# Kernel tuning notes

Hardware: AMD Instinct MI355X
Metric: run time of the kernel (lower is better)

Reference implementation:

```python
import jax, jax.numpy as jnp
import numpy as np

LSTM = 400      # lstm_size
K_ATT = 10      # attention_mixture_components
M_OUT = 20      # output_mixture_components
ALPHA = 60      # alphabet_size
B, T, TC = 64, 600, 50


def setup_inputs() -> dict:
    key = jax.random.key(0)
    ks = jax.random.split(key, 16)
    s = 0.05  # weight init scale to keep activations sane
    rn = lambda k, shape: (jax.random.normal(k, shape, jnp.float32) * s)
    d1 = 3 + ALPHA                # lstm1 input: [window, x]
    d2 = 3 + LSTM + ALPHA         # lstm2 input: [x, h1, window]
    d3 = 3 + 2 * LSTM + ALPHA     # lstm3 input: [x, h1, h2, window]
    H4 = 4 * LSTM
    return {
        "inputs": jax.random.normal(ks[0], (B, T, 3), jnp.float32),
        "char_seq": jax.random.randint(ks[1], (B, TC), 0, ALPHA),
        "char_seq_lengths": jax.random.randint(ks[2], (B,), 1, TC + 1),
        "W_ih1": rn(ks[3], (H4, d1)), "b_ih1": jnp.zeros((H4,), jnp.float32),
        "W_hh1": rn(ks[4], (H4, LSTM)), "b_hh1": jnp.zeros((H4,), jnp.float32),
        "W_ih2": rn(ks[5], (H4, d2)), "b_ih2": jnp.zeros((H4,), jnp.float32),
        "W_hh2": rn(ks[6], (H4, LSTM)), "b_hh2": jnp.zeros((H4,), jnp.float32),
        "W_ih3": rn(ks[7], (H4, d3)), "b_ih3": jnp.zeros((H4,), jnp.float32),
        "W_hh3": rn(ks[8], (H4, LSTM)), "b_hh3": jnp.zeros((H4,), jnp.float32),
        "W_att": rn(ks[9], (3 * K_ATT, LSTM)), "b_att": jnp.zeros((3 * K_ATT,), jnp.float32),
        "W_gmm": rn(ks[10], (6 * M_OUT + 1, 3 * LSTM)), "b_gmm": jnp.zeros((6 * M_OUT + 1,), jnp.float32),
    }


def _lstm_cell(x, h, c, Wih, bih, Whh, bhh):
    # torch.nn.LSTMCell gate order: i, f, g, o
    g = x @ Wih.T + bih + h @ Whh.T + bhh
    i, f, gg, o = jnp.split(g, 4, axis=-1)
    c_new = jax.nn.sigmoid(f) * c + jax.nn.sigmoid(i) * jnp.tanh(gg)
    h_new = jax.nn.sigmoid(o) * jnp.tanh(c_new)
    return h_new, c_new


def reference(inputs, char_seq, char_seq_lengths,
              W_ih1, b_ih1, W_hh1, b_hh1,
              W_ih2, b_ih2, W_hh2, b_hh2,
              W_ih3, b_ih3, W_hh3, b_hh3,
              W_att, b_att, W_gmm, b_gmm):
    M = M_OUT
    char_oh = jax.nn.one_hot(char_seq, ALPHA, dtype=inputs.dtype)       # [B,TC,A]
    u = jnp.arange(TC, dtype=inputs.dtype)                              # [TC]
    len_mask = (u[None, :] < char_seq_lengths[:, None].astype(inputs.dtype)).astype(inputs.dtype)  # [B,TC]

    def step(carry, x_t):
        h1, c1, h2, c2, h3, c3, window, kappa = carry
        # lstm1([window, x])
        h1, c1 = _lstm_cell(jnp.concatenate([window, x_t], -1), h1, c1, W_ih1, b_ih1, W_hh1, b_hh1)
        # Graves Gaussian-mixture attention window (no softmax)
        p = jnp.exp(h1 @ W_att.T + b_att)                               # [B,3K]
        alpha, beta, dkappa = jnp.split(p, 3, axis=-1)
        kappa = kappa + dkappa                                          # [B,K]
        diff = kappa[:, :, None] - u[None, None, :]                     # [B,K,TC]
        phi = jnp.sum(alpha[:, :, None] * jnp.exp(-beta[:, :, None] * diff * diff), axis=1)  # [B,TC]
        phi = phi * len_mask
        window = jnp.einsum('bt,bta->ba', phi, char_oh)                 # [B,A]
        # lstm2([x, h1, window]) / lstm3([x, h1, h2, window])
        h2, c2 = _lstm_cell(jnp.concatenate([x_t, h1, window], -1), h2, c2, W_ih2, b_ih2, W_hh2, b_hh2)
        h3, c3 = _lstm_cell(jnp.concatenate([x_t, h1, h2, window], -1), h3, c3, W_ih3, b_ih3, W_hh3, b_hh3)
        # GMM output layer (bias=None -> 0)
        z = jnp.concatenate([h1, h2, h3], -1) @ W_gmm.T + b_gmm          # [B,6M+1]
        e_hat = z[:, :1]
        pi_hat = z[:, 1:1 + M]
        mus = z[:, 1 + M:1 + 3 * M]
        sig_hat = z[:, 1 + 3 * M:1 + 5 * M]
        rho_hat = z[:, 1 + 5 * M:1 + 6 * M]
        out = jnp.concatenate([
            jax.nn.softmax(pi_hat, axis=-1),   # pis   [B,M]
            mus,                               # mus   [B,2M]
            jnp.exp(sig_hat),                  # sigmas[B,2M]
            jnp.tanh(rho_hat),                 # rhos  [B,M]
            jax.nn.sigmoid(e_hat),             # es    [B,1]
        ], axis=-1)
        return (h1, c1, h2, c2, h3, c3, window, kappa), out

    z0 = jnp.zeros((B, LSTM), inputs.dtype)
    carry0 = (z0, z0, z0, z0, z0, z0,
              jnp.zeros((B, ALPHA), inputs.dtype),
              jnp.zeros((B, K_ATT), inputs.dtype))
    _, outs = jax.lax.scan(step, carry0, jnp.swapaxes(inputs, 0, 1))    # [T,B,6M+1]
    return jnp.transpose(outs, (1, 0, 2))                               # [B,T,6M+1]
```

## Files before the change

### kernel.cpp

```cpp
#include <hip/hip_runtime.h>
#include <hip/hip_bf16.h>

#define NB 64
#define NT 600
#define NTC 50
#define NH 400
#define NKATT 10
#define NALPHA 60
#define NOUT 121

typedef unsigned short u16;
typedef _Float16 f16x2 __attribute__((ext_vector_type(2)));
typedef _Float16 f16x4 __attribute__((ext_vector_type(4)));
typedef _Float16 f16x8 __attribute__((ext_vector_type(8)));

#if defined(__has_builtin)
#if __has_builtin(__builtin_amdgcn_fdot2)
#define FDOT2(a,b,c) __builtin_amdgcn_fdot2((a),(b),(c),false)
#endif
#endif
#ifndef FDOT2
#define FDOT2(a,b,c) ((c) + (float)(a)[0]*(float)(b)[0] + (float)(a)[1]*(float)(b)[1])
#endif

#define ROWSP 1664

#define T1N 13
#define CGRP 15

#define H1R 0
#define H2R 102400
#define H3R 204800
#define WINR 256000
#define ST_FLOATS 271360
#define SLOT_H 25600
#define SLOT_W 3840

#define OF_WATT 0
#define OF_INB1 25600
#define OF_INB2 33792
#define OF_ACCS 48128
#define OF_AB   52736
#define OF_PHI  53696
#define OF_KAP  55296
#define OF_CHS  55616
#define OF_LEN  57216
#define OF_C1   57248
#define OF_C2   58272
#define SMEM_TOTAL 59296

__device__ __align__(16) f16x2 g_WT1[256 * ROWSP];
__device__ __align__(16) f16x2 g_WT2[448 * ROWSP];
__device__ __align__(16) f16x2 g_WT3[640 * ROWSP];
__device__ __align__(16) f16x2 g_WG8[150 * 128 * 4];
__device__ __align__(16) f16x2 g_WattP[200 * 32];
__device__ __align__(16) float g_fb1[ROWSP], g_fb2[ROWSP], g_fb3[ROWSP];
__device__ float g_batt[30], g_bgmm[121];
__device__ __align__(16) float g_inp[115200];
__device__ __align__(16) float g_state[ST_FLOATS];
__device__ unsigned int g_cnt[8 * 4 * 32];
__device__ int g_isf32;

#define CNT_A 0
#define CNT_B 1
#define CNT_C 2

__device__ __forceinline__ float bf2f(u16 v) {
    union { unsigned int u; float f; } t; t.u = ((unsigned int)v) << 16; return t.f;
}
__device__ __forceinline__ u16 f2bf(float f) {
    union { float ff; unsigned int u; } t; t.ff = f;
    unsigned int lsb = (t.u >> 16) & 1u;
    t.u += 0x7fffu + lsb;
    return (u16)(t.u >> 16);
}
__device__ __forceinline__ float sigm(float x) { return 1.f / (1.f + expf(-x)); }
__device__ __forceinline__ f16x2 packpair(float a, float b) {
    f16x2 r; r[0] = (_Float16)a; r[1] = (_Float16)b; return r;
}

__device__ __forceinline__ void st_agent(float* p, float v) {
    __hip_atomic_store(p, v, __ATOMIC_RELAXED, __HIP_MEMORY_SCOPE_AGENT);
}
__device__ __forceinline__ float2 ld2_agent(const float* p) {
    unsigned long long u = __hip_atomic_load((const unsigned long long*)p,
                                             __ATOMIC_RELAXED, __HIP_MEMORY_SCOPE_AGENT);
    union { unsigned long long u; float2 f; } t; t.u = u; return t.f;
}
__device__ __forceinline__ unsigned ld_cnt(int bg, int cid) {
    return __hip_atomic_load(&g_cnt[(bg * 4 + cid) * 32], __ATOMIC_RELAXED, __HIP_MEMORY_SCOPE_AGENT);
}
__device__ __forceinline__ void cnt_bump(int bg, int cid) {
    if (threadIdx.x == 0)
        __hip_atomic_fetch_add(&g_cnt[(bg * 4 + cid) * 32], 1u, __ATOMIC_RELAXED, __HIP_MEMORY_SCOPE_AGENT);
}
__device__ __forceinline__ void cnt_wait(int bg, int cid, unsigned tgt) {
    if (threadIdx.x == 0 && tgt > 0) {
        while (ld_cnt(bg, cid) < tgt) __builtin_amdgcn_s_sleep(1);
    }
    __syncthreads();
}

__global__ void k_detect(const void* whh1) {
    if (threadIdx.x == 0 && blockIdx.x == 0) {
        const u16* p = (const u16*)whh1;
        int f32 = 0;
        for (int k = 0; k < 256; ++k) {
            float v = bf2f(p[2 * k]);
            if (!(fabsf(v) < 1e3f)) f32 = 1;
        }
        g_isf32 = f32;
    }
}

__global__ void k_convert(const void* inp,
                          const void* wih1, const void* bih1, const void* whh1, const void* bhh1,
                          const void* wih2, const void* bih2, const void* whh2, const void* bhh2,
                          const void* wih3, const void* bih3, const void* whh3, const void* bhh3,
                          const void* watt, const void* batt, const void* wgmm, const void* bgmm)
{
    const int gt = blockIdx.x * blockDim.x + threadIdx.x;
    const int gs = gridDim.x * blockDim.x;
    const int f32 = g_isf32;
    auto ld = [f32](const void* p, int i) -> float {
        return f32 ? ((const float*)p)[i] : bf2f(((const u16*)p)[i]);
    };
    auto w1col = [&](int kf, int row) -> float {
        if (kf < 400) return ld(whh1, row * 400 + kf);
        if (kf < 460) return ld(wih1, row * 63 + (kf - 400));
        if (kf < 463) return ld(wih1, row * 63 + 60 + (kf - 460));
        return 0.f;
    };
    auto w2col = [&](int kf, int row) -> float {
        if (kf < 400) return ld(wih2, row * 463 + 3 + kf);
        if (kf < 800) return ld(whh2, row * 400 + (kf - 400));
        if (kf < 860) return ld(wih2, row * 463 + 403 + (kf - 800));
        if (kf < 863) return ld(wih2, row * 463 + (kf - 860));
        return 0.f;
    };
    auto w3col = [&](int kf, int row) -> float {
        if (kf < 400)  return ld(wih3, row * 863 + 3 + kf);
        if (kf < 800)  return ld(wih3, row * 863 + 403 + (kf - 400));
        if (kf < 1200) return ld(whh3, row * 400 + (kf - 800));
        if (kf < 1260) return ld(wih3, row * 863 + 803 + (kf - 1200));
        if (kf < 1263) return ld(wih3, row * 863 + (kf - 1260));
        return 0.f;
    };
    for (int i = gt; i < 256 * ROWSP; i += gs) {
        int k2 = i / ROWSP, rp = i % ROWSP;
        int j = rp >> 2, g = rp & 3;
        float a = 0.f, b = 0.f;
        if (j < 400) { int row = g * 400 + j; a = w1col(2 * k2, row); b = w1col(2 * k2 + 1, row); }
        g_WT1[i] = packpair(a, b);
    }
    for (int i = gt; i < 448 * ROWSP; i += gs) {
        int k2 = i / ROWSP, rp = i % ROWSP;
        int j = rp >> 2, g = rp & 3;
        float a = 0.f, b = 0.f;
        if (j < 400) { int row = g * 400 + j; a = w2col(2 * k2, row); b = w2col(2 * k2 + 1, row); }
        g_WT2[i] = packpair(a, b);
    }
    for (int i = gt; i < 640 * ROWSP; i += gs) {
        int k2 = i / ROWSP, rp = i % ROWSP;
        int j = rp >> 2, g = rp & 3;
        float a = 0.f, b = 0.f;
        if (j < 400) { int row = g * 400 + j; a = w3col(2 * k2, row); b = w3col(2 * k2 + 1, row); }
        g_WT3[i] = packpair(a, b);
    }
    for (int i = gt; i < ROWSP; i += gs) {
        int j = i >> 2, g = i & 3;
        float b1 = 0.f, b2 = 0.f, b3 = 0.f;
        if (j < 400) {
            int row = g * 400 + j;
            b1 = ld(bih1, row) + ld(bhh1, row);
            b2 = ld(bih2, row) + ld(bhh2, row);
            b3 = ld(bih3, row) + ld(bhh3, row);
        }
        g_fb1[i] = b1; g_fb2[i] = b2; g_fb3[i] = b3;
    }
    for (int i = gt; i < 200 * 32; i += gs) {
        int k2 = i / 32, r = i % 32;
        float a = 0.f, b = 0.f;
        if (r < 30) { a = ld(watt, r * 400 + 2 * k2); b = ld(watt, r * 400 + 2 * k2 + 1); }
        g_WattP[i] = packpair(a, b);
    }
    for (int i = gt; i < 150 * 128 * 4; i += gs) {
        int k8 = i >> 9, rem = i & 511, r = rem >> 2, j = rem & 3;
        int kp = k8 * 4 + j;
        float a = 0.f, b = 0.f;
        if (r < 121) { a = ld(wgmm, r * 1200 + 2 * kp); b = ld(wgmm, r * 1200 + 2 * kp + 1); }
        g_WG8[i] = packpair(a, b);
    }
    for (int i = gt; i < 30; i += gs)  g_batt[i] = ld(batt, i);
    for (int i = gt; i < 121; i += gs) g_bgmm[i] = ld(bgmm, i);
    for (int i = gt; i < 115200; i += gs) g_inp[i] = ld(inp, i);
    for (int i = gt; i < ST_FLOATS; i += gs) g_state[i] = 0.f;
    for (int i = gt; i < 8 * 4 * 32; i += gs) g_cnt[i] = 0u;
}

template<int KP2>
__device__ __forceinline__ void lstm_core(const f16x2* __restrict__ WT, const float* __restrict__ fb,
                                          float* __restrict__ cL, float* __restrict__ hdst,
                                          const f16x2* inb, float* accS, int rg, int bg, int tid)
{
    const int wv = tid >> 6, lane = tid & 63;
    const int ck4 = KP2 >> 5;
    const int k40 = wv * ck4;
    const int rbase = rg * 128 + lane * 2;
    float acc[2][8];
    #pragma unroll
    for (int r = 0; r < 2; ++r)
        #pragma unroll
        for (int b = 0; b < 8; ++b) acc[r][b] = 0.f;
    const f16x2* wp = WT + (size_t)(k40 * 4) * ROWSP + rbase;
    #pragma unroll 2
    for (int k4 = 0; k4 < ck4; ++k4) {
        f16x2 wa[4], wb[4];
        #pragma unroll
        for (int j = 0; j < 4; ++j) {
            union { f16x4 v; f16x2 p[2]; } u;
            u.v = *(const f16x4*)(wp + (size_t)j * ROWSP);
            wa[j] = u.p[0]; wb[j] = u.p[1];
        }
        #pragma unroll
        for (int b = 0; b < 8; ++b) {
            union { f16x8 v; f16x2 p[4]; } h;
            h.v = *(const f16x8*)(inb + b * KP2 + (k40 + k4) * 4);
            #pragma unroll
            for (int j = 0; j < 4; ++j) {
                acc[0][b] = FDOT2(wa[j], h.p[j], acc[0][b]);
                acc[1][b] = FDOT2(wb[j], h.p[j], acc[1][b]);
            }
        }
        wp += 4 * ROWSP;
    }
    #pragma unroll
    for (int r = 0; r < 2; ++r)
        #pragma unroll
        for (int b = 0; b < 8; ++b)
            atomicAdd(&accS[(lane * 2 + r) * 9 + b], acc[r][b]);
    __syncthreads();
    if (tid < 256) {
        int bl = tid >> 5, jj = tid & 31;
        int j = rg * 32 + jj;
        if (j < 400) {
            int rl = jj * 4;
            float gi = accS[(rl + 0) * 9 + bl] + fb[rg * 128 + rl + 0];
            float gf = accS[(rl + 1) * 9 + bl] + fb[rg * 128 + rl + 1];
            float gg = accS[(rl + 2) * 9 + bl] + fb[rg * 128 + rl + 2];
            float go = accS[(rl + 3) * 9 + bl] + fb[rg * 128 + rl + 3];
            float c = cL[bl * 32 + jj];
            float cn = sigm(gf) * c + sigm(gi) * tanhf(gg);
            cL[bl * 32 + jj] = cn;
            st_agent(&hdst[(bg * 8 + bl) * 400 + j], sigm(go) * tanhf(cn));
        }
    }
}

__device__ void out_head(void* out, int t, int obid, int tid, char* smem)
{
    f16x2* zb = (f16x2*)smem;
    float* zv = (float*)(smem + 9600);
    const float* h1 = g_state + H1R + (t & 3) * SLOT_H;
    const float* h2 = g_state + H2R + (t & 3) * SLOT_H;
    const float* h3 = g_state + H3R + (t & 1) * SLOT_H;
    for (int i = tid; i < 4 * 600; i += 512) {
        int bq = i / 600, p = i % 600; int b = obid * 4 + bq;
        int kf = 2 * p;
        const float* src = (kf < 400) ? (h1 + b * 400 + kf)
                         : (kf < 800) ? (h2 + b * 400 + (kf - 400))
                                      : (h3 + b * 400 + (kf - 800));
        float2 hv = ld2_agent(src);
        zb[bq * 600 + p] = packpair(hv.x, hv.y);
    }
    __syncthreads();
    {
        int bq = tid >> 7, r = tid & 127;
        float ac0 = (r < 121) ? g_bgmm[r] : 0.f, ac1 = 0.f, ac2 = 0.f, ac3 = 0.f;
        const f16x8* zp = (const f16x8*)(zb + bq * 600);
        #pragma unroll 4
        for (int k8 = 0; k8 < 150; ++k8) {
            union { f16x8 v; f16x2 p[4]; } w, z;
            w.v = *(const f16x8*)&g_WG8[(k8 * 128 + r) * 4];
            z.v = zp[k8];
            ac0 = FDOT2(w.p[0], z.p[0], ac0);
            ac1 = FDOT2(w.p[1], z.p[1], ac1);
            ac2 = FDOT2(w.p[2], z.p[2], ac2);
            ac3 = FDOT2(w.p[3], z.p[3], ac3);
        }
        if (r < 121) zv[bq * 121 + r] = (ac0 + ac1) + (ac2 + ac3);
    }
    __syncthreads();
    if (tid < 484) {
        int bl = tid / 121, jo = tid - bl * 121;
        const float* z = zv + bl * 121;
        float val;
        if (jo < 20) {
            float m = -1e30f;
            for (int i = 0; i < 20; ++i) m = fmaxf(m, z[1 + i]);
            float s = 0.f;
            for (int i = 0; i < 20; ++i) s += expf(z[1 + i] - m);
            val = expf(z[1 + jo] - m) / s;
        } else if (jo < 60)  val = z[jo + 1];
        else if (jo < 100)   val = expf(z[jo + 1]);
        else if (jo < 120)   val = tanhf(z[jo + 1]);
        else                 val = 1.f / (1.f + expf(-z[0]));
        int idx = ((obid * 4 + bl) * NT + t) * NOUT + jo;
        if (g_isf32) ((float*)out)[idx] = val;
        else         ((u16*)out)[idx]  = f2bf(val);
    }
    __syncthreads();
}

__global__ __launch_bounds__(512) void k_persist(void* out,
                                                 const int* __restrict__ cseq,
                                                 const int* __restrict__ clen)
{
    __shared__ __align__(16) char smem[SMEM_TOTAL];
    const int tid = threadIdx.x;
    const int bid = blockIdx.x;
    const int x = bid & 7, s = bid >> 3;
    int role, rg = 0, bg = 0, obid = 0;
    if (s < 8)       { role = 0; rg = x; bg = s; }
    else if (s < 13) { role = 0; int q = 5 * x + (s - 8);  rg = 8 + (q >> 3); bg = q & 7; }
    else if (s < 21) { role = 1; rg = x; bg = s - 13; }
    else if (s < 26) { role = 1; int q = 5 * x + (s - 21); rg = 8 + (q >> 3); bg = q & 7; }
    else             { role = 2; obid = 2 * x + (s - 26); bg = x; }

    if (role == 0) {
        f16x2* wattL = (f16x2*)(smem + OF_WATT);
        f16x2* inb1 = (f16x2*)(smem + OF_INB1);
        f16x2* inb2 = (f16x2*)(smem + OF_INB2);
        float* accS = (float*)(smem + OF_ACCS);
        float* ab  = (float*)(smem + OF_AB);
        float* phi = (float*)(smem + OF_PHI);
        float* kap = (float*)(smem + OF_KAP);
        int* chs = (int*)(smem + OF_CHS);
        int* len = (int*)(smem + OF_LEN);
        float* c1 = (float*)(smem + OF_C1);
        float* c2 = (float*)(smem + OF_C2);

        for (int i = tid; i < 200 * 32; i += 512) wattL[i] = g_WattP[i];
        for (int i = tid; i < 8 * 256; i += 512) inb1[i] = packpair(0.f, 0.f);
        for (int i = tid; i < 8 * 448; i += 512) inb2[i] = packpair(0.f, 0.f);
        for (int i = tid; i < 1152; i += 512) accS[i] = 0.f;
        if (tid < 80) kap[tid] = 0.f;
        if (tid >= 128 && tid < 384) { c1[tid - 128] = 0.f; c2[tid - 128] = 0.f; }
        for (int i = tid; i < 400; i += 512) chs[i] = cseq[(bg * 8 + i / 50) * NTC + i % 50];
        if (tid >= 384 && tid < 392) len[tid - 384] = clen[bg * 8 + (tid - 384)];
        if (tid < 16) {
            int bl = tid >> 1, hh = tid & 1, b = bg * 8 + bl;
            if (hh == 0) inb1[bl * 256 + 230] = packpair(g_inp[(b * NT) * 3 + 0], g_inp[(b * NT) * 3 + 1]);
            else         inb1[bl * 256 + 231] = packpair(g_inp[(b * NT) * 3 + 2], 0.f);
        }
        __syncthreads();
        lstm_core<256>(g_WT1, g_fb1, c1, g_state + H1R + 0 * SLOT_H, inb1, accS, rg, bg, tid);
        __syncthreads();
        cnt_bump(bg, CNT_A);

        for (int t = 0; t <= NT; ++t) {
            if (t >= 1) {
                for (int i = tid; i < 8 * 230; i += 512) {
                    int bl = i / 230, p = i - bl * 230;
                    inb2[bl * 448 + (p < 200 ? p : p + 200)] = inb1[bl * 256 + p];
                }
                if (tid < 16) {
                    int bl = tid >> 1, hh = tid & 1, b = bg * 8 + bl;
                    if (hh == 0) inb2[bl * 448 + 430] = packpair(g_inp[(b * NT + t - 1) * 3 + 0], g_inp[(b * NT + t - 1) * 3 + 1]);
                    else         inb2[bl * 448 + 431] = packpair(g_inp[(b * NT + t - 1) * 3 + 2], 0.f);
                }
                for (int i = tid; i < 1152; i += 512) accS[i] = 0.f;
                cnt_wait(bg, CNT_B, 13u * (unsigned)(t - 1));
                const float* h2s = g_state + H2R + ((t - 2) & 3) * SLOT_H;
                for (int i = tid; i < 8 * 200; i += 512) {
                    int bl = i / 200, p = i - bl * 200, b = bg * 8 + bl;
                    float2 hv = ld2_agent(h2s + b * 400 + 2 * p);
                    inb2[bl * 448 + 200 + p] = packpair(hv.x, hv.y);
                }
                __syncthreads();
                lstm_core<448>(g_WT2, g_fb2, c2, g_state + H2R + ((t - 1) & 3) * SLOT_H, inb2, accS, rg, bg, tid);
                __syncthreads();
                cnt_bump(bg, CNT_B);
                if (t == NT) break;
            }
            if (tid == 0) {
                unsigned tgtA = 13u * (unsigned)(t + 1);
                while (ld_cnt(bg, CNT_A) < tgtA) __builtin_amdgcn_s_sleep(1);
                if (t >= 2) {
                    unsigned tgtC = 15u * (unsigned)(t - 1);
                    while (ld_cnt(bg, CNT_C) < tgtC) __builtin_amdgcn_s_sleep(1);
                }
            }
            __syncthreads();
            const float* h1s = g_state + H1R + (t & 3) * SLOT_H;
            for (int i = tid; i < 8 * 200; i += 512) {
                int bl = i / 200, p = i - bl * 200, b = bg * 8 + bl;
                float2 hv = ld2_agent(h1s + b * 400 + 2 * p);
                inb1[bl * 256 + p] = packpair(hv.x, hv.y);
            }
            __syncthreads();
            if (tid < 240) {
                int bl = tid / 30, rr = tid - bl * 30;
                float a0 = g_batt[rr], a1 = 0.f;
                const f16x2* hp = inb1 + bl * 256;
                #pragma unroll 4
                for (int k2 = 0; k2 < 200; k2 += 2) {
                    a0 = FDOT2(wattL[(k2 + 0) * 32 + rr], hp[k2 + 0], a0);
                    a1 = FDOT2(wattL[(k2 + 1) * 32 + rr], hp[k2 + 1], a1);
                }
                ab[bl * 30 + rr] = expf(a0 + a1);
            }
            __syncthreads();
            if (tid < 400) {
                int bl = tid / 50, u = tid - bl * 50;
                float ph = 0.f;
                if (u < len[bl]) {
                    float uf = (float)u;
                    for (int k = 0; k < 10; ++k) {
                        float kn = kap[bl * 10 + k] + ab[bl * 30 + 20 + k];
                        float d = kn - uf;
                        ph += ab[bl * 30 + k] * expf(-ab[bl * 30 + 10 + k] * d * d);
                    }
                }
                phi[bl * 50 + u] = ph;
            }
            __syncthreads();
            if (tid < 240) {
                int bl = tid / 30, q = tid - bl * 30;
                int a0i = 2 * q, a1i = 2 * q + 1;
                float w0 = 0.f, w1 = 0.f;
                for (int u = 0; u < NTC; ++u) {
                    float pv = phi[bl * 50 + u]; int cc = chs[bl * 50 + u];
                    if (cc == a0i) w0 += pv;
                    if (cc == a1i) w1 += pv;
                }
                inb1[bl * 256 + 200 + q] = packpair(w0, w1);
                if (rg == 0) {
                    float* wr = g_state + WINR + (t & 3) * SLOT_W + (bg * 8 + bl) * 60;
                    st_agent(wr + a0i, w0); st_agent(wr + a1i, w1);
                }
            } else if (tid >= 256 && tid < 336) {
                int i = tid - 256; int bl = i / 10, k = i - bl * 10;
                kap[bl * 10 + k] += ab[bl * 30 + 20 + k];
            }
            if (t + 1 < NT && tid < 16) {
                int bl = tid >> 1, hh = tid & 1, b = bg * 8 + bl;
                if (hh == 0) inb1[bl * 256 + 230] = packpair(g_inp[(b * NT + t + 1) * 3 + 0], g_inp[(b * NT + t + 1) * 3 + 1]);
                else         inb1[bl * 256 + 231] = packpair(g_inp[(b * NT + t + 1) * 3 + 2], 0.f);
            }
            __syncthreads();
            if (t + 1 < NT) {
                for (int i = tid; i < 1152; i += 512) accS[i] = 0.f;
                __syncthreads();
                lstm_core<256>(g_WT1, g_fb1, c1, g_state + H1R + ((t + 1) & 3) * SLOT_H, inb1, accS, rg, bg, tid);
                __syncthreads();
                cnt_bump(bg, CNT_A);
            }
        }
    } else if (role == 1) {
        f16x2* inb3 = (f16x2*)smem;
        float* accS = (float*)(smem + 20480);
        float* c3 = (float*)(smem + 25088);
        for (int i = tid; i < 8 * 640; i += 512) inb3[i] = packpair(0.f, 0.f);
        if (tid < 256) c3[tid] = 0.f;
        __syncthreads();
        for (int t = 0; t < NT; ++t) {
            if (tid < 16) {
                int bl = tid >> 1, hh = tid & 1, b = bg * 8 + bl;
                if (hh == 0) inb3[bl * 640 + 630] = packpair(g_inp[(b * NT + t) * 3 + 0], g_inp[(b * NT + t) * 3 + 1]);
                else         inb3[bl * 640 + 631] = packpair(g_inp[(b * NT + t) * 3 + 2], 0.f);
            }
            for (int i = tid; i < 1152; i += 512) accS[i] = 0.f;
            cnt_wait(bg, CNT_B, 13u * (unsigned)(t + 1));
            const float* h1s = g_state + H1R + (t & 3) * SLOT_H;
            const float* h2s = g_state + H2R + (t & 3) * SLOT_H;
            const float* h3s = g_state + H3R + ((t - 1) & 1) * SLOT_H;
            const float* ws  = g_state + WINR + (t & 3) * SLOT_W;
            for (int i = tid; i < 8 * 630; i += 512) {
                int bl = i / 630, p = i - bl * 630, b = bg * 8 + bl;
                const float* src = (p < 200) ? h1s + b * 400 + 2 * p
                                 : (p < 400) ? h2s + b * 400 + 2 * (p - 200)
                                 : (p < 600) ? h3s + b * 400 + 2 * (p - 400)
                                             : ws  + b * 60  + 2 * (p - 600);
                float2 hv = ld2_agent(src);
                inb3[bl * 640 + p] = packpair(hv.x, hv.y);
            }
            __syncthreads();
            lstm_core<640>(g_WT3, g_fb3, c3, g_state + H3R + (t & 1) * SLOT_H, inb3, accS, rg, bg, tid);
            __syncthreads();
            cnt_bump(bg, CNT_C);
            cnt_wait(bg, CNT_C, 15u * (unsigned)(t + 1));
        }
    } else {
        for (int t = 0; t < NT; ++t) {
            cnt_bump(bg, CNT_C);
            cnt_wait(bg, CNT_C, 15u * (unsigned)(t + 1));
            out_head(out, t, obid, tid, smem);
        }
    }
}

extern "C" void kernel_launch(void* const* d_in, const int* in_sizes, int n_in,
                              void* d_out, int out_size, void* d_ws, size_t ws_size,
                              hipStream_t stream)
{
    hipLaunchKernelGGL(k_detect, dim3(1), dim3(64), 0, stream, d_in[5]);
    hipLaunchKernelGGL(k_convert, dim3(2048), dim3(256), 0, stream,
                       d_in[0],
                       d_in[3], d_in[4], d_in[5], d_in[6],
                       d_in[7], d_in[8], d_in[9], d_in[10],
                       d_in[11], d_in[12], d_in[13], d_in[14],
                       d_in[15], d_in[16], d_in[17], d_in[18]);
    void* outp = d_out;
    const int* cseq = (const int*)d_in[1];
    const int* clen = (const int*)d_in[2];
    void* args[] = { (void*)&outp, (void*)&cseq, (void*)&clen };
    hipLaunchCooperativeKernel((void*)k_persist, dim3(224), dim3(512), args, 0, stream);
}
```

Baseline: 25.31 ms.

## Move LSTM2 to role-1 blocks and recompute attention window redundantly

Role-0 blocks now run only LSTM1 plus attention. Role-1 blocks run LSTM2 and LSTM3 in sequence, recomputing the attention window locally instead of reading it from global memory. The h3 buffer widens to four slots, and role 1 drops its wait on the output head, so stages are more decoupled and LSTM1 can run further ahead. The cost is duplicated attention work in every role-1 block (which reads W_att from global rather than shared memory), and each role-1 block now does two LSTM layers serially per step.

Result: slower. 32.16 ms (+27.1%).

```diff
diff --git a/kernel.cpp b/kernel.cpp
--- a/kernel.cpp
+++ b/kernel.cpp
@@ -25,29 +25,32 @@
 
 #define ROWSP 1664
 
-#define T1N 13
-#define CGRP 15
-
 #define H1R 0
 #define H2R 102400
 #define H3R 204800
-#define WINR 256000
-#define ST_FLOATS 271360
+#define ST_FLOATS 307200
 #define SLOT_H 25600
-#define SLOT_W 3840
-
-#define OF_WATT 0
-#define OF_INB1 25600
-#define OF_INB2 33792
-#define OF_ACCS 48128
-#define OF_AB   52736
-#define OF_PHI  53696
-#define OF_KAP  55296
-#define OF_CHS  55616
-#define OF_LEN  57216
-#define OF_C1   57248
-#define OF_C2   58272
-#define SMEM_TOTAL 59296
+
+#define OF1_WATT 0
+#define OF1_INB1 25600
+#define OF1_ACCS 33792
+#define OF1_AB   38400
+#define OF1_PHI  39360
+#define OF1_KAP  40960
+#define OF1_CHS  41280
+#define OF1_LEN  42880
+#define OF1_C1   42912
+#define OF2_INB2 0
+#define OF2_INB3 14336
+#define OF2_ACCS 34816
+#define OF2_AB   39424
+#define OF2_PHI  40384
+#define OF2_KAP  41984
+#define OF2_CHS  42304
+#define OF2_LEN  43904
+#define OF2_C2   43936
+#define OF2_C3   44960
+#define SMEM_TOTAL 46080
 
 __device__ __align__(16) f16x2 g_WT1[256 * ROWSP];
 __device__ __align__(16) f16x2 g_WT2[448 * ROWSP];
@@ -257,13 +260,61 @@
     }
 }
 
+template<int STR, int WOFF>
+__device__ __forceinline__ void att_window(const f16x2* __restrict__ watt,
+                                           f16x2* inb, float* ab, float* phi, float* kap,
+                                           const int* chs, const int* len, int tid)
+{
+    if (tid < 240) {
+        int bl = tid / 30, rr = tid - bl * 30;
+        float a0 = g_batt[rr], a1 = 0.f;
+        const f16x2* hp = inb + bl * STR;
+        #pragma unroll 4
+        for (int k2 = 0; k2 < 200; k2 += 2) {
+            a0 = FDOT2(watt[(k2 + 0) * 32 + rr], hp[k2 + 0], a0);
+            a1 = FDOT2(watt[(k2 + 1) * 32 + rr], hp[k2 + 1], a1);
+        }
+        ab[bl * 30 + rr] = expf(a0 + a1);
+    }
+    __syncthreads();
+    if (tid < 400) {
+        int bl = tid / 50, u = tid - bl * 50;
+        float ph = 0.f;
+        if (u < len[bl]) {
+            float uf = (float)u;
+            for (int k = 0; k < 10; ++k) {
+                float kn = kap[bl * 10 + k] + ab[bl * 30 + 20 + k];
+                float d = kn - uf;
+                ph += ab[bl * 30 + k] * expf(-ab[bl * 30 + 10 + k] * d * d);
+            }
+        }
+        phi[bl * 50 + u] = ph;
+    }
+    __syncthreads();
+    if (tid < 240) {
+        int bl = tid / 30, q = tid - bl * 30;
+        int a0i = 2 * q, a1i = 2 * q + 1;
+        float w0 = 0.f, w1 = 0.f;
+        for (int u = 0; u < NTC; ++u) {
+            float pv = phi[bl * 50 + u]; int cc = chs[bl * 50 + u];
+            if (cc == a0i) w0 += pv;
+            if (cc == a1i) w1 += pv;
+        }
+        inb[bl * STR + WOFF + q] = packpair(w0, w1);
+    } else if (tid >= 256 && tid < 336) {
+        int i = tid - 256; int bl = i / 10, k = i - bl * 10;
+        kap[bl * 10 + k] += ab[bl * 30 + 20 + k];
+    }
+    __syncthreads();
+}
+
 __device__ void out_head(void* out, int t, int obid, int tid, char* smem)
 {
     f16x2* zb = (f16x2*)smem;
     float* zv = (float*)(smem + 9600);
     const float* h1 = g_state + H1R + (t & 3) * SLOT_H;
     const float* h2 = g_state + H2R + (t & 3) * SLOT_H;
-    const float* h3 = g_state + H3R + (t & 1) * SLOT_H;
+    const float* h3 = g_state + H3R + (t & 3) * SLOT_H;
     for (int i = tid; i < 4 * 600; i += 512) {
         int bq = i / 600, p = i % 600; int b = obid * 4 + bq;
         int kf = 2 * p;
@@ -328,24 +379,21 @@
     else             { role = 2; obid = 2 * x + (s - 26); bg = x; }
 
     if (role == 0) {
-        f16x2* wattL = (f16x2*)(smem + OF_WATT);
-        f16x2* inb1 = (f16x2*)(smem + OF_INB1);
-        f16x2* inb2 = (f16x2*)(smem + OF_INB2);
-        float* accS = (float*)(smem + OF_ACCS);
-        float* ab  = (float*)(smem + OF_AB);
-        float* phi = (float*)(smem + OF_PHI);
-        float* kap = (float*)(smem + OF_KAP);
-        int* chs = (int*)(smem + OF_CHS);
-        int* len = (int*)(smem + OF_LEN);
-        float* c1 = (float*)(smem + OF_C1);
-        float* c2 = (float*)(smem + OF_C2);
+        f16x2* wattL = (f16x2*)(smem + OF1_WATT);
+        f16x2* inb1 = (f16x2*)(smem + OF1_INB1);
+        float* accS = (float*)(smem + OF1_ACCS);
+        float* ab  = (float*)(smem + OF1_AB);
+        float* phi = (float*)(smem + OF1_PHI);
+        float* kap = (float*)(smem + OF1_KAP);
+        int* chs = (int*)(smem + OF1_CHS);
+        int* len = (int*)(smem + OF1_LEN);
+        float* c1 = (float*)(smem + OF1_C1);
 
         for (int i = tid; i < 200 * 32; i += 512) wattL[i] = g_WattP[i];
         for (int i = tid; i < 8 * 256; i += 512) inb1[i] = packpair(0.f, 0.f);
-        for (int i = tid; i < 8 * 448; i += 512) inb2[i] = packpair(0.f, 0.f);
         for (int i = tid; i < 1152; i += 512) accS[i] = 0.f;
         if (tid < 80) kap[tid] = 0.f;
-        if (tid >= 128 && tid < 384) { c1[tid - 128] = 0.f; c2[tid - 128] = 0.f; }
+        if (tid >= 128 && tid < 384) c1[tid - 128] = 0.f;
         for (int i = tid; i < 400; i += 512) chs[i] = cseq[(bg * 8 + i / 50) * NTC + i % 50];
         if (tid >= 384 && tid < 392) len[tid - 384] = clen[bg * 8 + (tid - 384)];
         if (tid < 16) {
@@ -358,36 +406,18 @@
         __syncthreads();
         cnt_bump(bg, CNT_A);
 
-        for (int t = 0; t <= NT; ++t) {
-            if (t >= 1) {
-                for (int i = tid; i < 8 * 230; i += 512) {
-                    int bl = i / 230, p = i - bl * 230;
-                    inb2[bl * 448 + (p < 200 ? p : p + 200)] = inb1[bl * 256 + p];
-                }
-                if (tid < 16) {
-                    int bl = tid >> 1, hh = tid & 1, b = bg * 8 + bl;
-                    if (hh == 0) inb2[bl * 448 + 430] = packpair(g_inp[(b * NT + t - 1) * 3 + 0], g_inp[(b * NT + t - 1) * 3 + 1]);
-                    else         inb2[bl * 448 + 431] = packpair(g_inp[(b * NT + t - 1) * 3 + 2], 0.f);
-                }
-                for (int i = tid; i < 1152; i += 512) accS[i] = 0.f;
-                cnt_wait(bg, CNT_B, 13u * (unsigned)(t - 1));
-                const float* h2s = g_state + H2R + ((t - 2) & 3) * SLOT_H;
-                for (int i = tid; i < 8 * 200; i += 512) {
-                    int bl = i / 200, p = i - bl * 200, b = bg * 8 + bl;
-                    float2 hv = ld2_agent(h2s + b * 400 + 2 * p);
-                    inb2[bl * 448 + 200 + p] = packpair(hv.x, hv.y);
-                }
-                __syncthreads();
-                lstm_core<448>(g_WT2, g_fb2, c2, g_state + H2R + ((t - 1) & 3) * SLOT_H, inb2, accS, rg, bg, tid);
-                __syncthreads();
-                cnt_bump(bg, CNT_B);
-                if (t == NT) break;
-            }
+        for (int t = 0; t < NT; ++t) {
+            if (t + 1 < NT && tid < 16) {
+                int bl = tid >> 1, hh = tid & 1, b = bg * 8 + bl;
+                if (hh == 0) inb1[bl * 256 + 230] = packpair(g_inp[(b * NT + t + 1) * 3 + 0], g_inp[(b * NT + t + 1) * 3 + 1]);
+                else         inb1[bl * 256 + 231] = packpair(g_inp[(b * NT + t + 1) * 3 + 2], 0.f);
+            }
+            for (int i = tid; i < 1152; i += 512) accS[i] = 0.f;
             if (tid == 0) {
                 unsigned tgtA = 13u * (unsigned)(t + 1);
                 while (ld_cnt(bg, CNT_A) < tgtA) __builtin_amdgcn_s_sleep(1);
-                if (t >= 2) {
-                    unsigned tgtC = 15u * (unsigned)(t - 1);
+                if (t >= 3) {
+                    unsigned tgtC = 15u * (unsigned)(t - 2);
                     while (ld_cnt(bg, CNT_C) < tgtC) __builtin_amdgcn_s_sleep(1);
                 }
             }
@@ -399,97 +429,79 @@
                 inb1[bl * 256 + p] = packpair(hv.x, hv.y);
             }
             __syncthreads();
-            if (tid < 240) {
-                int bl = tid / 30, rr = tid - bl * 30;
-                float a0 = g_batt[rr], a1 = 0.f;
-                const f16x2* hp = inb1 + bl * 256;
-                #pragma unroll 4
-                for (int k2 = 0; k2 < 200; k2 += 2) {
-                    a0 = FDOT2(wattL[(k2 + 0) * 32 + rr], hp[k2 + 0], a0);
-                    a1 = FDOT2(wattL[(k2 + 1) * 32 + rr], hp[k2 + 1], a1);
-                }
-                ab[bl * 30 + rr] = expf(a0 + a1);
-            }
-            __syncthreads();
-            if (tid < 400) {
-                int bl = tid / 50, u = tid - bl * 50;
-                float ph = 0.f;
-                if (u < len[bl]) {
-                    float uf = (float)u;
-                    for (int k = 0; k < 10; ++k) {
-                        float kn = kap[bl * 10 + k] + ab[bl * 30 + 20 + k];
-                        float d = kn - uf;
-                        ph += ab[bl * 30 + k] * expf(-ab[bl * 30 + 10 + k] * d * d);
-                    }
-                }
-                phi[bl * 50 + u] = ph;
-            }
-            __syncthreads();
-            if (tid < 240) {
-                int bl = tid / 30, q = tid - bl * 30;
-                int a0i = 2 * q, a1i = 2 * q + 1;
-                float w0 = 0.f, w1 = 0.f;
-                for (int u = 0; u < NTC; ++u) {
-                    float pv = phi[bl * 50 + u]; int cc = chs[bl * 50 + u];
-                    if (cc == a0i) w0 += pv;
-                    if (cc == a1i) w1 += pv;
-                }
-                inb1[bl * 256 + 200 + q] = packpair(w0, w1);
-                if (rg == 0) {
-                    float* wr = g_state + WINR + (t & 3) * SLOT_W + (bg * 8 + bl) * 60;
-                    st_agent(wr + a0i, w0); st_agent(wr + a1i, w1);
-                }
-            } else if (tid >= 256 && tid < 336) {
-                int i = tid - 256; int bl = i / 10, k = i - bl * 10;
-                kap[bl * 10 + k] += ab[bl * 30 + 20 + k];
-            }
-            if (t + 1 < NT && tid < 16) {
-                int bl = tid >> 1, hh = tid & 1, b = bg * 8 + bl;
-                if (hh == 0) inb1[bl * 256 + 230] = packpair(g_inp[(b * NT + t + 1) * 3 + 0], g_inp[(b * NT + t + 1) * 3 + 1]);
-                else         inb1[bl * 256 + 231] = packpair(g_inp[(b * NT + t + 1) * 3 + 2], 0.f);
-            }
-            __syncthreads();
+            att_window<256, 200>(wattL, inb1, ab, phi, kap, chs, len, tid);
             if (t + 1 < NT) {
-                for (int i = tid; i < 1152; i += 512) accS[i] = 0.f;
-                __syncthreads();
                 lstm_core<256>(g_WT1, g_fb1, c1, g_state + H1R + ((t + 1) & 3) * SLOT_H, inb1, accS, rg, bg, tid);
                 __syncthreads();
                 cnt_bump(bg, CNT_A);
             }
         }
     } else if (role == 1) {
-        f16x2* inb3 = (f16x2*)smem;
-        float* accS = (float*)(smem + 20480);
-        float* c3 = (float*)(smem + 25088);
+        f16x2* inb2 = (f16x2*)(smem + OF2_INB2);
+        f16x2* inb3 = (f16x2*)(smem + OF2_INB3);
+        float* accS = (float*)(smem + OF2_ACCS);
+        float* ab  = (float*)(smem + OF2_AB);
+        float* phi = (float*)(smem + OF2_PHI);
+        float* kap = (float*)(smem + OF2_KAP);
+        int* chs = (int*)(smem + OF2_CHS);
+        int* len = (int*)(smem + OF2_LEN);
+        float* c2 = (float*)(smem + OF2_C2);
+        float* c3 = (float*)(smem + OF2_C3);
+
+        for (int i = tid; i < 8 * 448; i += 512) inb2[i] = packpair(0.f, 0.f);
         for (int i = tid; i < 8 * 640; i += 512) inb3[i] = packpair(0.f, 0.f);
-        if (tid < 256) c3[tid] = 0.f;
+        if (tid < 80) kap[tid] = 0.f;
+        if (tid >= 128 && tid < 384) { c2[tid - 128] = 0.f; c3[tid - 128] = 0.f; }
+        for (int i = tid; i < 400; i += 512) chs[i] = cseq[(bg * 8 + i / 50) * NTC + i % 50];
+        if (tid >= 384 && tid < 392) len[tid - 384] = clen[bg * 8 + (tid - 384)];
         __syncthreads();
+
         for (int t = 0; t < NT; ++t) {
             if (tid < 16) {
                 int bl = tid >> 1, hh = tid & 1, b = bg * 8 + bl;
-                if (hh == 0) inb3[bl * 640 + 630] = packpair(g_inp[(b * NT + t) * 3 + 0], g_inp[(b * NT + t) * 3 + 1]);
-                else         inb3[bl * 640 + 631] = packpair(g_inp[(b * NT + t) * 3 + 2], 0.f);
+                if (hh == 0) inb2[bl * 448 + 430] = packpair(g_inp[(b * NT + t) * 3 + 0], g_inp[(b * NT + t) * 3 + 1]);
+                else         inb2[bl * 448 + 431] = packpair(g_inp[(b * NT + t) * 3 + 2], 0.f);
+            }
+            for (int i = tid; i < 8 * 200; i += 512) {
+                int bl = i / 200, p = i - bl * 200;
+                inb2[bl * 448 + 200 + p] = inb3[bl * 640 + 200 + p];
+            }
+            for (int i = tid; i < 1152; i += 512) accS[i] = 0.f;
+            cnt_wait(bg, CNT_A, 13u * (unsigned)(t + 1));
+            const float* h1s = g_state + H1R + (t & 3) * SLOT_H;
+            for (int i = tid; i < 8 * 200; i += 512) {
+                int bl = i / 200, p = i - bl * 200, b = bg * 8 + bl;
+                float2 hv = ld2_agent(h1s + b * 400 + 2 * p);
+                inb2[bl * 448 + p] = packpair(hv.x, hv.y);
+            }
+            __syncthreads();
+            att_window<448, 400>((const f16x2*)g_WattP, inb2, ab, phi, kap, chs, len, tid);
+            lstm_core<448>(g_WT2, g_fb2, c2, g_state + H2R + (t & 3) * SLOT_H, inb2, accS, rg, bg, tid);
+            __syncthreads();
+            cnt_bump(bg, CNT_B);
+            for (int i = tid; i < 8 * 232; i += 512) {
+                int bl = i / 232, j = i - bl * 232;
+                int src, dst;
+                if (j < 200)      { src = j;              dst = j; }
+                else if (j < 230) { src = 400 + (j - 200); dst = 600 + (j - 200); }
+                else              { src = 430 + (j - 230); dst = 630 + (j - 230); }
+                inb3[bl * 640 + dst] = inb2[bl * 448 + src];
             }
             for (int i = tid; i < 1152; i += 512) accS[i] = 0.f;
             cnt_wait(bg, CNT_B, 13u * (unsigned)(t + 1));
-            const float* h1s = g_state + H1R + (t & 3) * SLOT_H;
             const float* h2s = g_state + H2R + (t & 3) * SLOT_H;
-            const float* h3s = g_state + H3R + ((t - 1) & 1) * SLOT_H;
-            const float* ws  = g_state + WINR + (t & 3) * SLOT_W;
-            for (int i = tid; i < 8 * 630; i += 512) {
-                int bl = i / 630, p = i - bl * 630, b = bg * 8 + bl;
-                const float* src = (p < 200) ? h1s + b * 400 + 2 * p
-                                 : (p < 400) ? h2s + b * 400 + 2 * (p - 200)
-                                 : (p < 600) ? h3s + b * 400 + 2 * (p - 400)
-                                             : ws  + b * 60  + 2 * (p - 600);
+            const float* h3s = g_state + H3R + ((t - 1) & 3) * SLOT_H;
+            for (int i = tid; i < 8 * 400; i += 512) {
+                int bl = i / 400, p = i - bl * 400, b = bg * 8 + bl;
+                const float* src = (p < 200) ? h2s + b * 400 + 2 * p
+                                             : h3s + b * 400 + 2 * (p - 200);
                 float2 hv = ld2_agent(src);
-                inb3[bl * 640 + p] = packpair(hv.x, hv.y);
+                inb3[bl * 640 + 200 + p] = packpair(hv.x, hv.y);
             }
             __syncthreads();
-            lstm_core<640>(g_WT3, g_fb3, c3, g_state + H3R + (t & 1) * SLOT_H, inb3, accS, rg, bg, tid);
+            lstm_core<640>(g_WT3, g_fb3, c3, g_state + H3R + (t & 3) * SLOT_H, inb3, accS, rg, bg, tid);
             __syncthreads();
             cnt_bump(bg, CNT_C);
-            cnt_wait(bg, CNT_C, 15u * (unsigned)(t + 1));
         }
     } else {
         for (int t = 0; t < NT; ++t) {
```
